# Optimization experiments

Hardware: AMD Instinct MI355X
Metric: run time of the kernel (lower is better)

Reference implementation:

```python
import jax, jax.numpy as jnp
import numpy as np

H = 8
SPLIT = 1
# deterministic stand-in for random.shuffle(range(8)) in the original
_PERM = np.random.RandomState(0).permutation(H)
SERIES_IDX = jnp.asarray(_PERM[SPLIT:])  # 7 heads
CROSS_IDX = jnp.asarray(_PERM[:SPLIT])   # 1 head


def setup_inputs() -> dict:
    key = jax.random.key(0)
    ks = jax.random.split(key, 5)
    B, L, E = 8, 1024, 64
    shp = (B, L, H, E)
    return {
        "queries": jax.random.normal(ks[0], shp, dtype=jnp.float32),
        "keys": jax.random.normal(ks[1], shp, dtype=jnp.float32),
        "keysT": jax.random.normal(ks[2], shp, dtype=jnp.float32),
        "values": jax.random.normal(ks[3], shp, dtype=jnp.float32),
        "valuesT": jax.random.normal(ks[4], shp, dtype=jnp.float32),
    }


def reference(queries, keys, keysT, values, valuesT):
    B, L, _, E = queries.shape
    scale = 1.0 / jnp.sqrt(jnp.asarray(E, dtype=queries.dtype))
    neg_inf = jnp.asarray(-jnp.inf, dtype=queries.dtype)

    # head split (gather along head dim)
    sq = queries[:, :, SERIES_IDX]   # [B,L,7,E]
    sk = keys[:, :, SERIES_IDX]      # [B,S,7,E]
    sv = values[:, :, SERIES_IDX]    # [B,S,7,D]
    cq = queries[:, :, CROSS_IDX]    # [B,L,1,E]
    ckT = keysT[:, :, CROSS_IDX]     # [B,C,1,E]
    cvT = valuesT[:, :, CROSS_IDX]   # [B,C,1,D]

    # causal mask: True above the diagonal -> disallowed
    causal = jnp.triu(jnp.ones((L, L), dtype=bool), k=1)  # [L,L]

    # series branch
    scores = jnp.einsum('blne,bsne->bnls', sq, sk)  # [B,7,L,S]
    scores = jnp.where(causal[None, None], neg_inf, scores * scale)
    series = jax.nn.softmax(scores, axis=-1)
    V = jnp.einsum('bhls,bshd->blhd', series, sv)   # [B,L,7,D]

    # cross branch
    cscores = jnp.einsum('blme,bcme->bmlc', cq, ckT)  # [B,1,L,C]
    cscores = jnp.where(causal[None, None], neg_inf, cscores * scale)
    crosses = jax.nn.softmax(cscores, axis=-1)
    V_cross = jnp.einsum('bhlc,bchd->blhd', crosses, cvT)  # [B,L,1,D]

    return jnp.concatenate([V, V_cross], axis=2)  # [B,L,8,D]
```

## Files before the change

kernel.cpp:

```cpp
#include <hip/hip_runtime.h>
#include <math.h>

#define Lq 1024
#define Hq 8
#define Eq 64
#define LDW 72
#define KV_SH (64 * LDW)
#define BUF_SH (2 * KV_SH)

#define SRC_HEAD_PACKED 0x64503712u

typedef __bf16 bf16_t;
typedef __bf16 bf16x8 __attribute__((ext_vector_type(8)));
typedef __bf16 bf16x4 __attribute__((ext_vector_type(4)));
typedef short short4v __attribute__((ext_vector_type(4)));
typedef float floatx4 __attribute__((ext_vector_type(4)));

__device__ __forceinline__ bf16x8 cvt8(const float4 a, const float4 b) {
    bf16x8 r;
    r[0] = (bf16_t)a.x; r[1] = (bf16_t)a.y; r[2] = (bf16_t)a.z; r[3] = (bf16_t)a.w;
    r[4] = (bf16_t)b.x; r[5] = (bf16_t)b.y; r[6] = (bf16_t)b.z; r[7] = (bf16_t)b.w;
    return r;
}

__device__ __forceinline__ void block_sync_lds() {
    asm volatile("s_waitcnt lgkmcnt(0)" ::: "memory");
    __builtin_amdgcn_s_barrier();
    __builtin_amdgcn_sched_barrier(0);
}

__global__ __launch_bounds__(256, 2)
void attn_mfma(const float* __restrict__ Q, const float* __restrict__ Ks,
               const float* __restrict__ KTs, const float* __restrict__ Vs,
               const float* __restrict__ VTs, float* __restrict__ out) {
    const int slot = blockIdx.x;
    const int b    = blockIdx.y;
    const int p    = blockIdx.z;
    const int h    = (SRC_HEAD_PACKED >> (slot * 4)) & 0xF;
    const float* __restrict__ Kp = (slot == 7) ? KTs : Ks;
    const float* __restrict__ Vp = (slot == 7) ? VTs : Vs;
    const int pA = p, pB = 15 - p;

    const int tid  = threadIdx.x;
    const int wv   = tid >> 6;
    const int lane = tid & 63;
    const int ln16 = lane & 15;
    const int quad = lane >> 4;
    const int tb   = wv >> 1;
    const int kh   = wv & 1;
    const int pT   = tb ? pB : pA;

    __shared__ alignas(16) unsigned short smem[2 * BUF_SH];

    const float qs = 0.125f * 1.44269504f;
    bf16x8 qf[4][2];
    #pragma unroll
    for (int qg = 0; qg < 4; ++qg) {
        const int r = pT * 64 + qg * 16 + ln16;
        const float* qa = Q + (((size_t)b * Lq + r) * Hq + h) * Eq + quad * 8;
        #pragma unroll
        for (int ec = 0; ec < 2; ++ec) {
            float4 f0 = ((const float4*)(qa + ec * 32))[0];
            float4 f1 = ((const float4*)(qa + ec * 32))[1];
            f0.x*=qs; f0.y*=qs; f0.z*=qs; f0.w*=qs;
            f1.x*=qs; f1.y*=qs; f1.z*=qs; f1.w*=qs;
            qf[qg][ec] = cvt8(f0, f1);
        }
    }

    floatx4 O[4][4];
    #pragma unroll
    for (int qg = 0; qg < 4; ++qg)
        #pragma unroll
        for (int dc = 0; dc < 4; ++dc) O[qg][dc] = (floatx4){0, 0, 0, 0};
    float mq[4] = {-1e30f, -1e30f, -1e30f, -1e30f};
    float lq[4] = {0.f, 0.f, 0.f, 0.f};

    float4 kq[4];
    float  vq[16];
    const int kj = tid >> 2, kc = (tid & 3) * 16;
    const int vd = lane,     vk = wv * 16;

    auto load_tile = [&](int kt) {
        const float* kb = Kp + (((size_t)b * Lq + kt * 64 + kj) * Hq + h) * Eq + kc;
        kq[0] = ((const float4*)kb)[0]; kq[1] = ((const float4*)kb)[1];
        kq[2] = ((const float4*)kb)[2]; kq[3] = ((const float4*)kb)[3];
        const float* vb = Vp + (((size_t)b * Lq + kt * 64 + vk) * Hq + h) * Eq + vd;
        #pragma unroll
        for (int i = 0; i < 16; ++i) vq[i] = vb[(size_t)i * (Hq * Eq)];
    };
    auto stage = [&](int bsel) {
        unsigned short* dst = smem + bsel * BUF_SH;
        *(bf16x8*)&dst[kj * LDW + kc]     = cvt8(kq[0], kq[1]);
        *(bf16x8*)&dst[kj * LDW + kc + 8] = cvt8(kq[2], kq[3]);
        const float4* vq4 = (const float4*)vq;
        *(bf16x8*)&dst[KV_SH + vd * LDW + vk]     = cvt8(vq4[0], vq4[1]);
        *(bf16x8*)&dst[KV_SH + vd * LDW + vk + 8] = cvt8(vq4[2], vq4[3]);
    };

    load_tile(0);
    stage(0);
    load_tile(1);
    block_sync_lds();

    for (int kt = 0; kt <= pB; ++kt) {
        const unsigned short* base = smem + (kt & 1) * BUF_SH;
        const bool act = (kt <= pT);

        bf16x8 kf[2][2];
        if (act) {
            #pragma unroll
            for (int c = 0; c < 2; ++c) {
                kf[c][0] = *(const bf16x8*)&base[((kh * 2 + c) * 16 + ln16) * LDW + quad * 8];
                kf[c][1] = *(const bf16x8*)&base[((kh * 2 + c) * 16 + ln16) * LDW + 32 + quad * 8];
            }
        }
        if (kt < pB) stage((kt + 1) & 1);
        if (kt + 1 < pB) load_tile(kt + 2);

        if (act) {
            bf16x4 va[4][2];
            #pragma unroll
            for (int dc = 0; dc < 4; ++dc)
                #pragma unroll
                for (int nc = 0; nc < 2; ++nc)
                    va[dc][nc] = *(const bf16x4*)&base[KV_SH + (dc * 16 + ln16) * LDW + kh * 32 + nc * 16 + quad * 4];

            const bool diag = (kt == pT);
            #pragma unroll
            for (int qg = 0; qg < 4; ++qg) {
                if (diag && kh && qg < 2) continue;

                floatx4 s[2];
                #pragma unroll
                for (int nc = 0; nc < 2; ++nc) {
                    floatx4 acc = (floatx4){0, 0, 0, 0};
                    acc = __builtin_amdgcn_mfma_f32_16x16x32_bf16(kf[nc][0], qf[qg][0], acc, 0, 0, 0);
                    acc = __builtin_amdgcn_mfma_f32_16x16x32_bf16(kf[nc][1], qf[qg][1], acc, 0, 0, 0);
                    s[nc] = acc;
                }
                if (diag) {
                    const int rin = qg * 16 + ln16;
                    #pragma unroll
                    for (int nc = 0; nc < 2; ++nc)
                        #pragma unroll
                        for (int r = 0; r < 4; ++r)
                            if (kh * 32 + nc * 16 + quad * 4 + r > rin) s[nc][r] = -INFINITY;
                }
                float mn = s[0][0];
                #pragma unroll
                for (int nc = 0; nc < 2; ++nc)
                    #pragma unroll
                    for (int r = 0; r < 4; ++r) mn = fmaxf(mn, s[nc][r]);
                mn = fmaxf(mn, __shfl_xor(mn, 16, 64));
                mn = fmaxf(mn, __shfl_xor(mn, 32, 64));
                mn = fmaxf(mn, mq[qg]);
                const float alpha = __builtin_amdgcn_exp2f(mq[qg] - mn);
                mq[qg] = mn;
                float ps = 0.f;
                float pv[2][4];
                #pragma unroll
                for (int nc = 0; nc < 2; ++nc)
                    #pragma unroll
                    for (int r = 0; r < 4; ++r) {
                        pv[nc][r] = __builtin_amdgcn_exp2f(s[nc][r] - mn);
                        ps += pv[nc][r];
                    }
                ps += __shfl_xor(ps, 16, 64);
                ps += __shfl_xor(ps, 32, 64);
                lq[qg] = lq[qg] * alpha + ps;
                #pragma unroll
                for (int dc = 0; dc < 4; ++dc) O[qg][dc] *= alpha;

                short4v pb[2];
                #pragma unroll
                for (int nc = 0; nc < 2; ++nc) {
                    bf16x4 t;
                    t[0] = (bf16_t)pv[nc][0]; t[1] = (bf16_t)pv[nc][1];
                    t[2] = (bf16_t)pv[nc][2]; t[3] = (bf16_t)pv[nc][3];
                    pb[nc] = __builtin_bit_cast(short4v, t);
                }
                #pragma unroll
                for (int dc = 0; dc < 4; ++dc)
                    #pragma unroll
                    for (int nc = 0; nc < 2; ++nc)
                        O[qg][dc] = __builtin_amdgcn_mfma_f32_16x16x16bf16_1k(
                            __builtin_bit_cast(short4v, va[dc][nc]), pb[nc], O[qg][dc], 0, 0, 0);
            }
        }
        block_sync_lds();
    }

    float* mb = (float*)smem + tb * 4608;
    if (kh) {
        #pragma unroll
        for (int qg = 0; qg < 4; ++qg) {
            float* dst = mb + (qg * 64 + lane) * 18;
            #pragma unroll
            for (int dc = 0; dc < 4; ++dc) {
                *(float2*)(dst + dc * 4)     = make_float2(O[qg][dc][0], O[qg][dc][1]);
                *(float2*)(dst + dc * 4 + 2) = make_float2(O[qg][dc][2], O[qg][dc][3]);
            }
            dst[16] = mq[qg]; dst[17] = lq[qg];
        }
    }
    __syncthreads();
    if (!kh) {
        #pragma unroll
        for (int qg = 0; qg < 4; ++qg) {
            const float* src = mb + (qg * 64 + lane) * 18;
            const float m1 = src[16], l1 = src[17];
            const float mm = fmaxf(mq[qg], m1);
            const float a0 = __builtin_amdgcn_exp2f(mq[qg] - mm);
            const float a1 = __builtin_amdgcn_exp2f(m1 - mm);
            const float inv = 1.0f / (lq[qg] * a0 + l1 * a1);
            const int row = pT * 64 + qg * 16 + ln16;
            float* op = out + (((size_t)b * Lq + row) * Hq + slot) * Eq + quad * 4;
            #pragma unroll
            for (int dc = 0; dc < 4; ++dc) {
                float4 o;
                o.x = (O[qg][dc][0] * a0 + src[dc * 4 + 0] * a1) * inv;
                o.y = (O[qg][dc][1] * a0 + src[dc * 4 + 1] * a1) * inv;
                o.z = (O[qg][dc][2] * a0 + src[dc * 4 + 2] * a1) * inv;
                o.w = (O[qg][dc][3] * a0 + src[dc * 4 + 3] * a1) * inv;
                *(float4*)(op + dc * 16) = o;
            }
        }
    }
}

extern "C" void kernel_launch(void* const* d_in, const int* in_sizes, int n_in,
                              void* d_out, int out_size, void* d_ws, size_t ws_size,
                              hipStream_t stream) {
    const float* queries = (const float*)d_in[0];
    const float* keys    = (const float*)d_in[1];
    const float* keysT   = (const float*)d_in[2];
    const float* values  = (const float*)d_in[3];
    const float* valuesT = (const float*)d_in[4];
    float* out = (float*)d_out;

    dim3 grid(Hq, 8, 8);
    dim3 block(256);
    attn_mfma<<<grid, block, 0, stream>>>(queries, keys, keysT, values, valuesT, out);
}
```

Measured before the change: 143.1 us.

## Replace paired causal query tiles with one query tile per block, heaviest first

New measurement: 133.9 us. 1.07x faster.

```diff
diff --git a/kernel.cpp b/kernel.cpp
--- a/kernel.cpp
+++ b/kernel.cpp
@@ -35,28 +35,27 @@
                const float* __restrict__ VTs, float* __restrict__ out) {
     const int slot = blockIdx.x;
     const int b    = blockIdx.y;
-    const int p    = blockIdx.z;
+    const int qt   = 15 - blockIdx.z;
     const int h    = (SRC_HEAD_PACKED >> (slot * 4)) & 0xF;
     const float* __restrict__ Kp = (slot == 7) ? KTs : Ks;
     const float* __restrict__ Vp = (slot == 7) ? VTs : Vs;
-    const int pA = p, pB = 15 - p;
 
     const int tid  = threadIdx.x;
     const int wv   = tid >> 6;
     const int lane = tid & 63;
     const int ln16 = lane & 15;
     const int quad = lane >> 4;
-    const int tb   = wv >> 1;
     const int kh   = wv & 1;
-    const int pT   = tb ? pB : pA;
+    const int wh   = wv >> 1;
 
     __shared__ alignas(16) unsigned short smem[2 * BUF_SH];
 
     const float qs = 0.125f * 1.44269504f;
-    bf16x8 qf[4][2];
+    bf16x8 qf[2][2];
     #pragma unroll
-    for (int qg = 0; qg < 4; ++qg) {
-        const int r = pT * 64 + qg * 16 + ln16;
+    for (int qi = 0; qi < 2; ++qi) {
+        const int qg = wh * 2 + qi;
+        const int r = qt * 64 + qg * 16 + ln16;
         const float* qa = Q + (((size_t)b * Lq + r) * Hq + h) * Eq + quad * 8;
         #pragma unroll
         for (int ec = 0; ec < 2; ++ec) {
@@ -64,17 +63,17 @@
             float4 f1 = ((const float4*)(qa + ec * 32))[1];
             f0.x*=qs; f0.y*=qs; f0.z*=qs; f0.w*=qs;
             f1.x*=qs; f1.y*=qs; f1.z*=qs; f1.w*=qs;
-            qf[qg][ec] = cvt8(f0, f1);
-        }
-    }
-
-    floatx4 O[4][4];
+            qf[qi][ec] = cvt8(f0, f1);
+        }
+    }
+
+    floatx4 O[2][4];
     #pragma unroll
-    for (int qg = 0; qg < 4; ++qg)
-        #pragma unroll
-        for (int dc = 0; dc < 4; ++dc) O[qg][dc] = (floatx4){0, 0, 0, 0};
-    float mq[4] = {-1e30f, -1e30f, -1e30f, -1e30f};
-    float lq[4] = {0.f, 0.f, 0.f, 0.f};
+    for (int qi = 0; qi < 2; ++qi)
+        #pragma unroll
+        for (int dc = 0; dc < 4; ++dc) O[qi][dc] = (floatx4){0, 0, 0, 0};
+    float mq[2] = {-1e30f, -1e30f};
+    float lq[2] = {0.f, 0.f};
 
     float4 kq[4];
     float  vq[16];
@@ -103,126 +102,124 @@
     load_tile(1);
     block_sync_lds();
 
-    for (int kt = 0; kt <= pB; ++kt) {
+    for (int kt = 0; kt <= qt; ++kt) {
         const unsigned short* base = smem + (kt & 1) * BUF_SH;
-        const bool act = (kt <= pT);
 
         bf16x8 kf[2][2];
-        if (act) {
-            #pragma unroll
-            for (int c = 0; c < 2; ++c) {
-                kf[c][0] = *(const bf16x8*)&base[((kh * 2 + c) * 16 + ln16) * LDW + quad * 8];
-                kf[c][1] = *(const bf16x8*)&base[((kh * 2 + c) * 16 + ln16) * LDW + 32 + quad * 8];
-            }
-        }
-        if (kt < pB) stage((kt + 1) & 1);
-        if (kt + 1 < pB) load_tile(kt + 2);
-
-        if (act) {
-            bf16x4 va[4][2];
-            #pragma unroll
-            for (int dc = 0; dc < 4; ++dc)
-                #pragma unroll
-                for (int nc = 0; nc < 2; ++nc)
-                    va[dc][nc] = *(const bf16x4*)&base[KV_SH + (dc * 16 + ln16) * LDW + kh * 32 + nc * 16 + quad * 4];
-
-            const bool diag = (kt == pT);
-            #pragma unroll
-            for (int qg = 0; qg < 4; ++qg) {
-                if (diag && kh && qg < 2) continue;
-
-                floatx4 s[2];
-                #pragma unroll
-                for (int nc = 0; nc < 2; ++nc) {
-                    floatx4 acc = (floatx4){0, 0, 0, 0};
-                    acc = __builtin_amdgcn_mfma_f32_16x16x32_bf16(kf[nc][0], qf[qg][0], acc, 0, 0, 0);
-                    acc = __builtin_amdgcn_mfma_f32_16x16x32_bf16(kf[nc][1], qf[qg][1], acc, 0, 0, 0);
-                    s[nc] = acc;
-                }
-                if (diag) {
-                    const int rin = qg * 16 + ln16;
-                    #pragma unroll
-                    for (int nc = 0; nc < 2; ++nc)
-                        #pragma unroll
-                        for (int r = 0; r < 4; ++r)
-                            if (kh * 32 + nc * 16 + quad * 4 + r > rin) s[nc][r] = -INFINITY;
-                }
-                float mn = s[0][0];
+        #pragma unroll
+        for (int c = 0; c < 2; ++c) {
+            kf[c][0] = *(const bf16x8*)&base[((kh * 2 + c) * 16 + ln16) * LDW + quad * 8];
+            kf[c][1] = *(const bf16x8*)&base[((kh * 2 + c) * 16 + ln16) * LDW + 32 + quad * 8];
+        }
+        if (kt < qt) stage((kt + 1) & 1);
+        if (kt + 1 < qt) load_tile(kt + 2);
+
+        bf16x4 va[4][2];
+        #pragma unroll
+        for (int dc = 0; dc < 4; ++dc)
+            #pragma unroll
+            for (int nc = 0; nc < 2; ++nc)
+                va[dc][nc] = *(const bf16x4*)&base[KV_SH + (dc * 16 + ln16) * LDW + kh * 32 + nc * 16 + quad * 4];
+
+        const bool diag = (kt == qt);
+        #pragma unroll
+        for (int qi = 0; qi < 2; ++qi) {
+            const int qg = wh * 2 + qi;
+            if (diag && kh && wh == 0) continue;
+
+            floatx4 s[2];
+            #pragma unroll
+            for (int nc = 0; nc < 2; ++nc) {
+                floatx4 acc = (floatx4){0, 0, 0, 0};
+                acc = __builtin_amdgcn_mfma_f32_16x16x32_bf16(kf[nc][0], qf[qi][0], acc, 0, 0, 0);
+                acc = __builtin_amdgcn_mfma_f32_16x16x32_bf16(kf[nc][1], qf[qi][1], acc, 0, 0, 0);
+                s[nc] = acc;
+            }
+            if (diag) {
+                const int rin = qg * 16 + ln16;
                 #pragma unroll
                 for (int nc = 0; nc < 2; ++nc)
                     #pragma unroll
-                    for (int r = 0; r < 4; ++r) mn = fmaxf(mn, s[nc][r]);
-                mn = fmaxf(mn, __shfl_xor(mn, 16, 64));
-                mn = fmaxf(mn, __shfl_xor(mn, 32, 64));
-                mn = fmaxf(mn, mq[qg]);
-                const float alpha = __builtin_amdgcn_exp2f(mq[qg] - mn);
-                mq[qg] = mn;
-                float ps = 0.f;
-                float pv[2][4];
+                    for (int r = 0; r < 4; ++r)
+                        if (kh * 32 + nc * 16 + quad * 4 + r > rin) s[nc][r] = -INFINITY;
+            }
+            float mn = s[0][0];
+            #pragma unroll
+            for (int nc = 0; nc < 2; ++nc)
+                #pragma unroll
+                for (int r = 0; r < 4; ++r) mn = fmaxf(mn, s[nc][r]);
+            mn = fmaxf(mn, __shfl_xor(mn, 16, 64));
+            mn = fmaxf(mn, __shfl_xor(mn, 32, 64));
+            mn = fmaxf(mn, mq[qi]);
+            const float alpha = __builtin_amdgcn_exp2f(mq[qi] - mn);
+            mq[qi] = mn;
+            float ps = 0.f;
+            float pv[2][4];
+            #pragma unroll
+            for (int nc = 0; nc < 2; ++nc)
+                #pragma unroll
+                for (int r = 0; r < 4; ++r) {
+                    pv[nc][r] = __builtin_amdgcn_exp2f(s[nc][r] - mn);
+                    ps += pv[nc][r];
+                }
+            ps += __shfl_xor(ps, 16, 64);
+            ps += __shfl_xor(ps, 32, 64);
+            lq[qi] = lq[qi] * alpha + ps;
+            #pragma unroll
+            for (int dc = 0; dc < 4; ++dc) O[qi][dc] *= alpha;
+
+            short4v pb[2];
+            #pragma unroll
+            for (int nc = 0; nc < 2; ++nc) {
+                bf16x4 t;
+                t[0] = (bf16_t)pv[nc][0]; t[1] = (bf16_t)pv[nc][1];
+                t[2] = (bf16_t)pv[nc][2]; t[3] = (bf16_t)pv[nc][3];
+                pb[nc] = __builtin_bit_cast(short4v, t);
+            }
+            #pragma unroll
+            for (int dc = 0; dc < 4; ++dc)
                 #pragma unroll
                 for (int nc = 0; nc < 2; ++nc)
-                    #pragma unroll
-                    for (int r = 0; r < 4; ++r) {
-                        pv[nc][r] = __builtin_amdgcn_exp2f(s[nc][r] - mn);
-                        ps += pv[nc][r];
-                    }
-                ps += __shfl_xor(ps, 16, 64);
-                ps += __shfl_xor(ps, 32, 64);
-                lq[qg] = lq[qg] * alpha + ps;
-                #pragma unroll
-                for (int dc = 0; dc < 4; ++dc) O[qg][dc] *= alpha;
-
-                short4v pb[2];
-                #pragma unroll
-                for (int nc = 0; nc < 2; ++nc) {
-                    bf16x4 t;
-                    t[0] = (bf16_t)pv[nc][0]; t[1] = (bf16_t)pv[nc][1];
-                    t[2] = (bf16_t)pv[nc][2]; t[3] = (bf16_t)pv[nc][3];
-                    pb[nc] = __builtin_bit_cast(short4v, t);
-                }
-                #pragma unroll
-                for (int dc = 0; dc < 4; ++dc)
-                    #pragma unroll
-                    for (int nc = 0; nc < 2; ++nc)
-                        O[qg][dc] = __builtin_amdgcn_mfma_f32_16x16x16bf16_1k(
-                            __builtin_bit_cast(short4v, va[dc][nc]), pb[nc], O[qg][dc], 0, 0, 0);
-            }
+                    O[qi][dc] = __builtin_amdgcn_mfma_f32_16x16x16bf16_1k(
+                        __builtin_bit_cast(short4v, va[dc][nc]), pb[nc], O[qi][dc], 0, 0, 0);
         }
         block_sync_lds();
     }
 
-    float* mb = (float*)smem + tb * 4608;
+    float* mb = (float*)smem;
     if (kh) {
         #pragma unroll
-        for (int qg = 0; qg < 4; ++qg) {
+        for (int qi = 0; qi < 2; ++qi) {
+            const int qg = wh * 2 + qi;
             float* dst = mb + (qg * 64 + lane) * 18;
             #pragma unroll
             for (int dc = 0; dc < 4; ++dc) {
-                *(float2*)(dst + dc * 4)     = make_float2(O[qg][dc][0], O[qg][dc][1]);
-                *(float2*)(dst + dc * 4 + 2) = make_float2(O[qg][dc][2], O[qg][dc][3]);
-            }
-            dst[16] = mq[qg]; dst[17] = lq[qg];
+                *(float2*)(dst + dc * 4)     = make_float2(O[qi][dc][0], O[qi][dc][1]);
+                *(float2*)(dst + dc * 4 + 2) = make_float2(O[qi][dc][2], O[qi][dc][3]);
+            }
+            dst[16] = mq[qi]; dst[17] = lq[qi];
         }
     }
     __syncthreads();
     if (!kh) {
         #pragma unroll
-        for (int qg = 0; qg < 4; ++qg) {
+        for (int qi = 0; qi < 2; ++qi) {
+            const int qg = wh * 2 + qi;
             const float* src = mb + (qg * 64 + lane) * 18;
             const float m1 = src[16], l1 = src[17];
-            const float mm = fmaxf(mq[qg], m1);
-            const float a0 = __builtin_amdgcn_exp2f(mq[qg] - mm);
+            const float mm = fmaxf(mq[qi], m1);
+            const float a0 = __builtin_amdgcn_exp2f(mq[qi] - mm);
             const float a1 = __builtin_amdgcn_exp2f(m1 - mm);
-            const float inv = 1.0f / (lq[qg] * a0 + l1 * a1);
-            const int row = pT * 64 + qg * 16 + ln16;
+            const float inv = 1.0f / (lq[qi] * a0 + l1 * a1);
+            const int row = qt * 64 + qg * 16 + ln16;
             float* op = out + (((size_t)b * Lq + row) * Hq + slot) * Eq + quad * 4;
             #pragma unroll
             for (int dc = 0; dc < 4; ++dc) {
                 float4 o;
-                o.x = (O[qg][dc][0] * a0 + src[dc * 4 + 0] * a1) * inv;
-                o.y = (O[qg][dc][1] * a0 + src[dc * 4 + 1] * a1) * inv;
-                o.z = (O[qg][dc][2] * a0 + src[dc * 4 + 2] * a1) * inv;
-                o.w = (O[qg][dc][3] * a0 + src[dc * 4 + 3] * a1) * inv;
+                o.x = (O[qi][dc][0] * a0 + src[dc * 4 + 0] * a1) * inv;
+                o.y = (O[qi][dc][1] * a0 + src[dc * 4 + 1] * a1) * inv;
+                o.z = (O[qi][dc][2] * a0 + src[dc * 4 + 2] * a1) * inv;
+                o.w = (O[qi][dc][3] * a0 + src[dc * 4 + 3] * a1) * inv;
                 *(float4*)(op + dc * 16) = o;
             }
         }
@@ -239,7 +236,7 @@
     const float* valuesT = (const float*)d_in[4];
     float* out = (float*)d_out;
 
-    dim3 grid(Hq, 8, 8);
+    dim3 grid(Hq, 8, 16);
     dim3 block(256);
     attn_mfma<<<grid, block, 0, stream>>>(queries, keys, keysT, values, valuesT, out);
 }
```
